# Performance work log

Hardware: AMD Instinct MI355X
Metric: run time of the kernel (lower is better)

## Reference

```python
import jax, jax.numpy as jnp
import numpy as np

B, N, D, H = 4, 512, 3, 128


def _linear_params(key, fan_in, fan_out):
    kw, kb = jax.random.split(key)
    lim = 1.0 / np.sqrt(fan_in)
    W = jax.random.uniform(kw, (fan_in, fan_out), jnp.float32, -lim, lim)
    b = jax.random.uniform(kb, (fan_out,), jnp.float32, -lim, lim)
    return W, b


def setup_inputs() -> dict:
    key = jax.random.key(0)
    ks = jax.random.split(key, 9)
    x = jax.random.normal(ks[0], (B, N, D), jnp.float32)
    Ws1, bs1 = _linear_params(ks[1], D, H)   # make_features.single
    Wp1, bp1 = _linear_params(ks[2], D, H)   # make_features.pair
    Wc1s, bc1s = _linear_params(ks[3], H, H)  # combine1.single
    Wc1p, bc1p = _linear_params(ks[4], H, H)  # combine1.pair
    Wpl, bpl = _linear_params(ks[5], H, H)    # pair_lin
    Wc2s, bc2s = _linear_params(ks[6], H, D)  # combine2.single (random, not zero-init, to exercise full graph)
    Wc2p, bc2p = _linear_params(ks[7], H, D)  # combine2.pair
    Wskip = -jnp.eye(D, dtype=jnp.float32)    # skip.weight init = -I (applied as x @ Wskip.T)
    return dict(x=x, Ws1=Ws1, bs1=bs1, Wp1=Wp1, bp1=bp1,
                Wc1s=Wc1s, bc1s=bc1s, Wc1p=Wc1p, bc1p=bc1p,
                Wpl=Wpl, bpl=bpl, Wc2s=Wc2s, bc2s=bc2s,
                Wc2p=Wc2p, bc2p=bc2p, Wskip=Wskip)


def reference(x, Ws1, bs1, Wp1, bp1, Wc1s, bc1s, Wc1p, bc1p,
              Wpl, bpl, Wc2s, bc2s, Wc2p, bc2p, Wskip):
    ht = lambda v: jnp.clip(v, -1.0, 1.0)  # Hardtanh
    n = x.shape[-2]
    # pairs[..., i, j, :] = x[j] - x[i]
    pairs = x[..., None, :, :] - x[..., :, None, :]          # [B, N, N, D]
    s = ht(x @ Ws1 + bs1)                                    # [B, N, H]
    p = ht(pairs @ Wp1 + bp1)                                # [B, N, N, H]
    # combine1: single(s) + pair(p).sum(dim=-3); sum-then-matmul is identical math, cheaper
    s = s @ Wc1s + bc1s + (p.sum(axis=-3) @ Wc1p + n * bc1p)  # [B, N, H]
    p = p @ Wpl + bpl                                         # [B, N, N, H]
    s = ht(s)
    p = ht(p)
    out = s @ Wc2s + bc2s + (p.sum(axis=-3) @ Wc2p + n * bc2p)  # [B, N, D]
    out = out + x @ Wskip.T                                     # skip (bias-free linear)
    return out
```

## Files before the change

kernel.cpp:

```cpp
#include <hip/hip_runtime.h>
#include <hip/hip_bf16.h>


typedef float f32x4 __attribute__((ext_vector_type(4)));
typedef __bf16 bf16x8 __attribute__((ext_vector_type(8)));

union PKU { uint4 u; bf16x8 v; };

__device__ __forceinline__ float ht1(float v) { return __builtin_amdgcn_fmed3f(v, -1.0f, 1.0f); }
__device__ __forceinline__ unsigned f2bf(float f) {
    unsigned u = __float_as_uint(f);
    u += 0x7FFF + ((u >> 16) & 1);
    return u >> 16;
}
__device__ __forceinline__ unsigned cvtpk(float a, float b) {
    unsigned r;
    asm("v_cvt_pk_bf16_f32 %0, %1, %2" : "=v"(r) : "v"(a), "v"(b));
    return r;
}

__global__ void prep_kernel(const float* __restrict__ x, const float* __restrict__ Wp1,
                            const float* __restrict__ Wpl,
                            const float* __restrict__ Wc1s, const float* __restrict__ Wc1p,
                            float* __restrict__ q, unsigned* __restrict__ wsBf,
                            float* __restrict__ wt1s, float* __restrict__ wt1p) {
    int gid = blockIdx.x * 256 + threadIdx.x;
    if (blockIdx.x < 1024) {
        int h = gid & 127, n = gid >> 7;
        const float* xp = x + n * 3;
        q[gid] = xp[0] * Wp1[h] + xp[1] * Wp1[128 + h] + xp[2] * Wp1[256 + h];
    } else if (blockIdx.x < 1056) {
        int g = gid - 1024 * 256;
        int w  = g & 3;
        int l  = (g >> 2) & 63;
        int fi = g >> 8;
        int wn = fi >> 4, nf = (fi >> 2) & 3, kf = fi & 3;
        int n = wn * 64 + nf * 16 + (l & 15);
        int k = kf * 32 + (l >> 4) * 8 + w * 2;
        unsigned lo = f2bf(Wpl[k * 128 + n]);
        unsigned hi = f2bf(Wpl[(k + 1) * 128 + n]);
        wsBf[g] = lo | (hi << 16);
    } else {
        int g = gid - 1056 * 256;
        int m = g >> 14;
        int e = g & 16383;
        int h = e >> 7, k = e & 127;
        if (m) wt1p[e] = Wc1p[k * 128 + h];
        else   wt1s[e] = Wc1s[k * 128 + h];
    }
}

__global__ __launch_bounds__(256, 2) void pair_kernel(
    const float* __restrict__ q, const unsigned* __restrict__ wsBf,
    const float* __restrict__ bp1, const float* __restrict__ bpl,
    const float* __restrict__ x,
    const float* __restrict__ Ws1, const float* __restrict__ bs1,
    const float* __restrict__ wt1s, const float* __restrict__ wt1p,
    const float* __restrict__ bc1s, const float* __restrict__ bc1p,
    const float* __restrict__ Wc2s, const float* __restrict__ bc2s,
    const float* __restrict__ Wc2p, const float* __restrict__ bc2p,
    const float* __restrict__ Wskip,
    float* __restrict__ out)
{
    __shared__ uint4 A_lds[2][2048];
    __shared__ float ps1[16][128];
    __shared__ float ps2[2][128];
    __shared__ float s1l[128], p1l[128], s2p[2][128], red[8];

    const int tid  = threadIdx.x;
    const int lane = tid & 63;
    const int wid  = tid >> 6;
    const int wm = wid >> 1, wn = wid & 1;
    const int bj = blockIdx.x;
    const int b  = bj >> 9;
    const float* __restrict__ qb = q + (b << 9) * 128;

    bf16x8 Bf[4][4];
    #pragma unroll
    for (int nf = 0; nf < 4; ++nf)
        #pragma unroll
        for (int kf = 0; kf < 4; ++kf) {
            PKU t;
            t.u = *(const uint4*)(wsBf + ((((wn << 4) | (nf << 2) | kf) << 6) | lane) * 4);
            Bf[nf][kf] = t.v;
        }

    const int c = tid & 15, rb = tid >> 4;
    float qjb[8];
    {
        const float* qj = q + bj * 128 + c * 8;
        #pragma unroll
        for (int e = 0; e < 8; ++e) qjb[e] = qj[e] + bp1[c * 8 + e];
    }
    float bplv[4];
    #pragma unroll
    for (int nf = 0; nf < 4; ++nf) bplv[nf] = bpl[wn * 64 + nf * 16 + (lane & 15)];

    float psum1r[8] = {0, 0, 0, 0, 0, 0, 0, 0};
    f32x4 acc[4][4];
    float colsum[4] = {0, 0, 0, 0};
    const f32x4 zf = (f32x4){0.f, 0.f, 0.f, 0.f};

    for (int ch = 0; ch < 4; ++ch) {
        uint4* __restrict__ Ab = A_lds[ch & 1];
        #pragma unroll
        for (int u = 0; u < 8; ++u) {
            const int r = (u << 4) | rb;
            const int i = (ch << 7) | r;
            const float4 q0 = *(const float4*)(qb + i * 128 + c * 8);
            const float4 q1 = *(const float4*)(qb + i * 128 + c * 8 + 4);
            float p[8];
            p[0] = ht1(qjb[0] - q0.x); p[1] = ht1(qjb[1] - q0.y);
            p[2] = ht1(qjb[2] - q0.z); p[3] = ht1(qjb[3] - q0.w);
            p[4] = ht1(qjb[4] - q1.x); p[5] = ht1(qjb[5] - q1.y);
            p[6] = ht1(qjb[6] - q1.z); p[7] = ht1(qjb[7] - q1.w);
            #pragma unroll
            for (int e = 0; e < 8; ++e) psum1r[e] += p[e];
            uint4 pk;
            pk.x = cvtpk(p[0], p[1]);
            pk.y = cvtpk(p[2], p[3]);
            pk.z = cvtpk(p[4], p[5]);
            pk.w = cvtpk(p[6], p[7]);
            unsigned addr = (r << 8) | (c << 4);
            addr ^= ((r & 7) << 4);
            Ab[addr >> 4] = pk;
        }
        __syncthreads();
        #pragma unroll
        for (int kf = 0; kf < 4; ++kf) {
            bf16x8 Af[4];
            #pragma unroll
            for (int mf = 0; mf < 4; ++mf) {
                const int row = wm * 64 + mf * 16 + (lane & 15);
                unsigned addr = (row << 8) + (kf << 6) + ((lane >> 4) << 4);
                addr ^= ((row & 7) << 4);
                PKU t; t.u = Ab[addr >> 4];
                Af[mf] = t.v;
            }
            #pragma unroll
            for (int mf = 0; mf < 4; ++mf)
                #pragma unroll
                for (int nf = 0; nf < 4; ++nf)
                    acc[mf][nf] = __builtin_amdgcn_mfma_f32_16x16x32_bf16(
                        Af[mf], Bf[nf][kf], kf == 0 ? zf : acc[mf][nf], 0, 0, 0);
        }
        #pragma unroll
        for (int mf = 0; mf < 4; ++mf)
            #pragma unroll
            for (int nf = 0; nf < 4; ++nf) {
                f32x4 a = acc[mf][nf];
                colsum[nf] += ht1(a.x + bplv[nf]) + ht1(a.y + bplv[nf])
                            + ht1(a.z + bplv[nf]) + ht1(a.w + bplv[nf]);
            }
    }

    *(float4*)(&ps1[rb][c * 8])     = make_float4(psum1r[0], psum1r[1], psum1r[2], psum1r[3]);
    *(float4*)(&ps1[rb][c * 8 + 4]) = make_float4(psum1r[4], psum1r[5], psum1r[6], psum1r[7]);
    #pragma unroll
    for (int nf = 0; nf < 4; ++nf) {
        float v = colsum[nf];
        v += __shfl_xor(v, 16);
        v += __shfl_xor(v, 32);
        if (lane < 16) ps2[wm][wn * 64 + nf * 16 + lane] = v;
    }
    __syncthreads();

    const int h = tid & 127;
    if (tid < 128) {
        float s = 0.f;
        #pragma unroll
        for (int r2 = 0; r2 < 16; ++r2) s += ps1[r2][tid];
        p1l[tid] = s;
        const float* xj = x + bj * 3;
        s1l[tid] = ht1(xj[0] * Ws1[tid] + xj[1] * Ws1[128 + tid] + xj[2] * Ws1[256 + tid] + bs1[tid]);
    }
    __syncthreads();

    {
        const int half = tid >> 7;
        const float* w1 = wt1s + h * 128 + half * 64;
        const float* w2 = wt1p + h * 128 + half * 64;
        float a2 = 0.f;
        #pragma unroll
        for (int k = 0; k < 64; k += 4) {
            float4 wa = *(const float4*)(w1 + k);
            float4 wb = *(const float4*)(w2 + k);
            const int kk = half * 64 + k;
            a2 += wa.x * s1l[kk] + wa.y * s1l[kk + 1] + wa.z * s1l[kk + 2] + wa.w * s1l[kk + 3];
            a2 += wb.x * p1l[kk] + wb.y * p1l[kk + 1] + wb.z * p1l[kk + 2] + wb.w * p1l[kk + 3];
        }
        s2p[half][h] = a2;
    }
    __syncthreads();

    if (tid < 128) {
        float s3 = ht1(s2p[0][tid] + s2p[1][tid] + bc1s[tid] + 512.0f * bc1p[tid]);
        float pp = ps2[0][tid] + ps2[1][tid];
        float c0 = s3 * Wc2s[tid * 3 + 0] + pp * Wc2p[tid * 3 + 0];
        float c1 = s3 * Wc2s[tid * 3 + 1] + pp * Wc2p[tid * 3 + 1];
        float c2 = s3 * Wc2s[tid * 3 + 2] + pp * Wc2p[tid * 3 + 2];
        #pragma unroll
        for (int off = 32; off > 0; off >>= 1) {
            c0 += __shfl_down(c0, off);
            c1 += __shfl_down(c1, off);
            c2 += __shfl_down(c2, off);
        }
        if (lane == 0) {
            red[wid * 3 + 0] = c0;
            red[wid * 3 + 1] = c1;
            red[wid * 3 + 2] = c2;
        }
    }
    __syncthreads();
    if (tid < 3) {
        const float* xj = x + bj * 3;
        float o = red[tid] + red[3 + tid];
        o += bc2s[tid] + 512.0f * bc2p[tid];
        o += xj[0] * Wskip[tid * 3 + 0] + xj[1] * Wskip[tid * 3 + 1] + xj[2] * Wskip[tid * 3 + 2];
        out[bj * 3 + tid] = o;
    }
}

extern "C" void kernel_launch(void* const* d_in, const int* in_sizes, int n_in,
                              void* d_out, int out_size, void* d_ws, size_t ws_size,
                              hipStream_t stream) {
    const float* x    = (const float*)d_in[0];
    const float* Ws1  = (const float*)d_in[1];
    const float* bs1  = (const float*)d_in[2];
    const float* Wp1  = (const float*)d_in[3];
    const float* bp1  = (const float*)d_in[4];
    const float* Wc1s = (const float*)d_in[5];
    const float* bc1s = (const float*)d_in[6];
    const float* Wc1p = (const float*)d_in[7];
    const float* bc1p = (const float*)d_in[8];
    const float* Wpl  = (const float*)d_in[9];
    const float* bpl  = (const float*)d_in[10];
    const float* Wc2s = (const float*)d_in[11];
    const float* bc2s = (const float*)d_in[12];
    const float* Wc2p = (const float*)d_in[13];
    const float* bc2p = (const float*)d_in[14];
    const float* Wskip= (const float*)d_in[15];

    float*    q    = (float*)d_ws;
    unsigned* wsBf = (unsigned*)((char*)d_ws + (1 << 20));
    float*    wt1s = (float*)((char*)d_ws + (1 << 20) + 32768);
    float*    wt1p = wt1s + 16384;

    prep_kernel<<<1184, 256, 0, stream>>>(x, Wp1, Wpl, Wc1s, Wc1p, q, wsBf, wt1s, wt1p);
    pair_kernel<<<2048, 256, 0, stream>>>(q, wsBf, bp1, bpl, x, Ws1, bs1,
                                          wt1s, wt1p, bc1s, bc1p,
                                          Wc2s, bc2s, Wc2p, bc2p, Wskip,
                                          (float*)d_out);
}
```

Before: 179.0 us.

## Single-buffer LDS in a union and raise pair kernel occupancy to four blocks

Shrinks LDS use of the pair kernel by replacing the double-buffered A tile with one buffer, adding a barrier after the MFMA reads so the next chunk can overwrite it. The reduction scratch arrays now share the same LDS space through a union, and the per-row psum partials are first reduced across lanes with shuffles so only four rows remain. Launch bounds are raised from 2 to 4 blocks per CU. The aim is more resident waves to hide latency, in exchange for an extra barrier per chunk and a tighter register budget that may cause spills.

```diff
diff --git a/kernel.cpp b/kernel.cpp
--- a/kernel.cpp
+++ b/kernel.cpp
@@ -50,7 +50,7 @@
     }
 }
 
-__global__ __launch_bounds__(256, 2) void pair_kernel(
+__global__ __launch_bounds__(256, 4) void pair_kernel(
     const float* __restrict__ q, const unsigned* __restrict__ wsBf,
     const float* __restrict__ bp1, const float* __restrict__ bpl,
     const float* __restrict__ x,
@@ -62,10 +62,16 @@
     const float* __restrict__ Wskip,
     float* __restrict__ out)
 {
-    __shared__ uint4 A_lds[2][2048];
-    __shared__ float ps1[16][128];
-    __shared__ float ps2[2][128];
-    __shared__ float s1l[128], p1l[128], s2p[2][128], red[8];
+    __shared__ union {
+        uint4 A[2048];
+        struct {
+            float ps1[4][128];
+            float ps2[2][128];
+            float s1l[128], p1l[128];
+            float s2p[2][128];
+            float red[8];
+        } t;
+    } sm;
 
     const int tid  = threadIdx.x;
     const int lane = tid & 63;
@@ -102,7 +108,6 @@
     const f32x4 zf = (f32x4){0.f, 0.f, 0.f, 0.f};
 
     for (int ch = 0; ch < 4; ++ch) {
-        uint4* __restrict__ Ab = A_lds[ch & 1];
         #pragma unroll
         for (int u = 0; u < 8; ++u) {
             const int r = (u << 4) | rb;
@@ -123,7 +128,7 @@
             pk.w = cvtpk(p[6], p[7]);
             unsigned addr = (r << 8) | (c << 4);
             addr ^= ((r & 7) << 4);
-            Ab[addr >> 4] = pk;
+            sm.A[addr >> 4] = pk;
         }
         __syncthreads();
         #pragma unroll
@@ -134,7 +139,7 @@
                 const int row = wm * 64 + mf * 16 + (lane & 15);
                 unsigned addr = (row << 8) + (kf << 6) + ((lane >> 4) << 4);
                 addr ^= ((row & 7) << 4);
-                PKU t; t.u = Ab[addr >> 4];
+                PKU t; t.u = sm.A[addr >> 4];
                 Af[mf] = t.v;
             }
             #pragma unroll
@@ -144,6 +149,7 @@
                     acc[mf][nf] = __builtin_amdgcn_mfma_f32_16x16x32_bf16(
                         Af[mf], Bf[nf][kf], kf == 0 ? zf : acc[mf][nf], 0, 0, 0);
         }
+        __syncthreads();
         #pragma unroll
         for (int mf = 0; mf < 4; ++mf)
             #pragma unroll
@@ -154,25 +160,29 @@
             }
     }
 
-    *(float4*)(&ps1[rb][c * 8])     = make_float4(psum1r[0], psum1r[1], psum1r[2], psum1r[3]);
-    *(float4*)(&ps1[rb][c * 8 + 4]) = make_float4(psum1r[4], psum1r[5], psum1r[6], psum1r[7]);
+    #pragma unroll
+    for (int e = 0; e < 8; ++e) {
+        psum1r[e] += __shfl_xor(psum1r[e], 16);
+        psum1r[e] += __shfl_xor(psum1r[e], 32);
+    }
+    if ((lane >> 4) == 0) {
+        *(float4*)(&sm.t.ps1[wid][c * 8])     = make_float4(psum1r[0], psum1r[1], psum1r[2], psum1r[3]);
+        *(float4*)(&sm.t.ps1[wid][c * 8 + 4]) = make_float4(psum1r[4], psum1r[5], psum1r[6], psum1r[7]);
+    }
     #pragma unroll
     for (int nf = 0; nf < 4; ++nf) {
         float v = colsum[nf];
         v += __shfl_xor(v, 16);
         v += __shfl_xor(v, 32);
-        if (lane < 16) ps2[wm][wn * 64 + nf * 16 + lane] = v;
+        if (lane < 16) sm.t.ps2[wm][wn * 64 + nf * 16 + lane] = v;
     }
     __syncthreads();
 
     const int h = tid & 127;
     if (tid < 128) {
-        float s = 0.f;
-        #pragma unroll
-        for (int r2 = 0; r2 < 16; ++r2) s += ps1[r2][tid];
-        p1l[tid] = s;
+        sm.t.p1l[tid] = sm.t.ps1[0][tid] + sm.t.ps1[1][tid] + sm.t.ps1[2][tid] + sm.t.ps1[3][tid];
         const float* xj = x + bj * 3;
-        s1l[tid] = ht1(xj[0] * Ws1[tid] + xj[1] * Ws1[128 + tid] + xj[2] * Ws1[256 + tid] + bs1[tid]);
+        sm.t.s1l[tid] = ht1(xj[0] * Ws1[tid] + xj[1] * Ws1[128 + tid] + xj[2] * Ws1[256 + tid] + bs1[tid]);
     }
     __syncthreads();
 
@@ -186,16 +196,16 @@
             float4 wa = *(const float4*)(w1 + k);
             float4 wb = *(const float4*)(w2 + k);
             const int kk = half * 64 + k;
-            a2 += wa.x * s1l[kk] + wa.y * s1l[kk + 1] + wa.z * s1l[kk + 2] + wa.w * s1l[kk + 3];
-            a2 += wb.x * p1l[kk] + wb.y * p1l[kk + 1] + wb.z * p1l[kk + 2] + wb.w * p1l[kk + 3];
-        }
-        s2p[half][h] = a2;
+            a2 += wa.x * sm.t.s1l[kk] + wa.y * sm.t.s1l[kk + 1] + wa.z * sm.t.s1l[kk + 2] + wa.w * sm.t.s1l[kk + 3];
+            a2 += wb.x * sm.t.p1l[kk] + wb.y * sm.t.p1l[kk + 1] + wb.z * sm.t.p1l[kk + 2] + wb.w * sm.t.p1l[kk + 3];
+        }
+        sm.t.s2p[half][h] = a2;
     }
     __syncthreads();
 
     if (tid < 128) {
-        float s3 = ht1(s2p[0][tid] + s2p[1][tid] + bc1s[tid] + 512.0f * bc1p[tid]);
-        float pp = ps2[0][tid] + ps2[1][tid];
+        float s3 = ht1(sm.t.s2p[0][tid] + sm.t.s2p[1][tid] + bc1s[tid] + 512.0f * bc1p[tid]);
+        float pp = sm.t.ps2[0][tid] + sm.t.ps2[1][tid];
         float c0 = s3 * Wc2s[tid * 3 + 0] + pp * Wc2p[tid * 3 + 0];
         float c1 = s3 * Wc2s[tid * 3 + 1] + pp * Wc2p[tid * 3 + 1];
         float c2 = s3 * Wc2s[tid * 3 + 2] + pp * Wc2p[tid * 3 + 2];
@@ -206,15 +216,15 @@
             c2 += __shfl_down(c2, off);
         }
         if (lane == 0) {
-            red[wid * 3 + 0] = c0;
-            red[wid * 3 + 1] = c1;
-            red[wid * 3 + 2] = c2;
+            sm.t.red[wid * 3 + 0] = c0;
+            sm.t.red[wid * 3 + 1] = c1;
+            sm.t.red[wid * 3 + 2] = c2;
         }
     }
     __syncthreads();
     if (tid < 3) {
         const float* xj = x + bj * 3;
-        float o = red[tid] + red[3 + tid];
+        float o = sm.t.red[tid] + sm.t.red[3 + tid];
         o += bc2s[tid] + 512.0f * bc2p[tid];
         o += xj[0] * Wskip[tid * 3 + 0] + xj[1] * Wskip[tid * 3 + 1] + xj[2] * Wskip[tid * 3 + 2];
         out[bj * 3 + tid] = o;
@@ -241,13 +251,13 @@
     const float* bc2p = (const float*)d_in[14];
     const float* Wskip= (const float*)d_in[15];
 
-    float*    q    = (float*)d_ws;
+    float*    qv   = (float*)d_ws;
     unsigned* wsBf = (unsigned*)((char*)d_ws + (1 << 20));
     float*    wt1s = (float*)((char*)d_ws + (1 << 20) + 32768);
     float*    wt1p = wt1s + 16384;
 
-    prep_kernel<<<1184, 256, 0, stream>>>(x, Wp1, Wpl, Wc1s, Wc1p, q, wsBf, wt1s, wt1p);
-    pair_kernel<<<2048, 256, 0, stream>>>(q, wsBf, bp1, bpl, x, Ws1, bs1,
+    prep_kernel<<<1184, 256, 0, stream>>>(x, Wp1, Wpl, Wc1s, Wc1p, qv, wsBf, wt1s, wt1p);
+    pair_kernel<<<2048, 256, 0, stream>>>(qv, wsBf, bp1, bpl, x, Ws1, bs1,
                                           wt1s, wt1p, bc1s, bc1p,
                                           Wc2s, bc2s, Wc2p, bc2p, Wskip,
                                           (float*)d_out);
```

Result: slower. 317.4 us (+77.4%).

## Build MFMA A-fragments directly in registers, removing LDS staging of pair features

Applied to the files above, without the earlier changes.

The pair-feature tile used to be written to shared memory as bf16 and read back as MFMA A operands, with block-wide barriers between chunks. Now each lane computes its own A fragment directly in the MFMA operand layout from q rows and feeds the bf16 MFMA without going through LDS, looping over 16-row tiles. This removes the LDS traffic, the swizzled stores and loads, and the per-chunk __syncthreads. In exchange, both wn waves in a pair recompute the same hardtanh and pack work, register pressure rises from the 4x8 qjb and psum arrays, and the first-layer row sums now need a shuffle reduction.

```diff
diff --git a/kernel.cpp b/kernel.cpp
--- a/kernel.cpp
+++ b/kernel.cpp
@@ -62,15 +62,18 @@
     const float* __restrict__ Wskip,
     float* __restrict__ out)
 {
-    __shared__ uint4 A_lds[2][2048];
-    __shared__ float ps1[16][128];
-    __shared__ float ps2[2][128];
-    __shared__ float s1l[128], p1l[128], s2p[2][128], red[8];
+    __shared__ float ps1s[2][128];
+    __shared__ float ps2s[2][128];
+    __shared__ float s1l[128], p1l[128];
+    __shared__ float s2p[2][128];
+    __shared__ float red[8];
 
     const int tid  = threadIdx.x;
     const int lane = tid & 63;
     const int wid  = tid >> 6;
     const int wm = wid >> 1, wn = wid & 1;
+    const int lr = lane & 15;
+    const int ls = lane >> 4;
     const int bj = blockIdx.x;
     const int b  = bj >> 9;
     const float* __restrict__ qb = q + (b << 9) * 128;
@@ -85,92 +88,107 @@
             Bf[nf][kf] = t.v;
         }
 
-    const int c = tid & 15, rb = tid >> 4;
-    float qjb[8];
-    {
-        const float* qj = q + bj * 128 + c * 8;
-        #pragma unroll
-        for (int e = 0; e < 8; ++e) qjb[e] = qj[e] + bp1[c * 8 + e];
-    }
-    float bplv[4];
-    #pragma unroll
-    for (int nf = 0; nf < 4; ++nf) bplv[nf] = bpl[wn * 64 + nf * 16 + (lane & 15)];
-
-    float psum1r[8] = {0, 0, 0, 0, 0, 0, 0, 0};
-    f32x4 acc[4][4];
+    float qjb[4][8];
+    #pragma unroll
+    for (int kf = 0; kf < 4; ++kf) {
+        const float4 a0 = *(const float4*)(q + bj * 128 + kf * 32 + ls * 8);
+        const float4 a1 = *(const float4*)(q + bj * 128 + kf * 32 + ls * 8 + 4);
+        const float4 b0 = *(const float4*)(bp1 + kf * 32 + ls * 8);
+        const float4 b1 = *(const float4*)(bp1 + kf * 32 + ls * 8 + 4);
+        qjb[kf][0] = a0.x + b0.x; qjb[kf][1] = a0.y + b0.y;
+        qjb[kf][2] = a0.z + b0.z; qjb[kf][3] = a0.w + b0.w;
+        qjb[kf][4] = a1.x + b1.x; qjb[kf][5] = a1.y + b1.y;
+        qjb[kf][6] = a1.z + b1.z; qjb[kf][7] = a1.w + b1.w;
+    }
+    float bplv4[4];
+    #pragma unroll
+    for (int nf = 0; nf < 4; ++nf) bplv4[nf] = bpl[wn * 64 + nf * 16 + lr];
+
+    float psum1r[4][8];
+    #pragma unroll
+    for (int kf = 0; kf < 4; ++kf)
+        #pragma unroll
+        for (int e = 0; e < 8; ++e) psum1r[kf][e] = 0.f;
     float colsum[4] = {0, 0, 0, 0};
     const f32x4 zf = (f32x4){0.f, 0.f, 0.f, 0.f};
 
-    for (int ch = 0; ch < 4; ++ch) {
-        uint4* __restrict__ Ab = A_lds[ch & 1];
-        #pragma unroll
-        for (int u = 0; u < 8; ++u) {
-            const int r = (u << 4) | rb;
-            const int i = (ch << 7) | r;
-            const float4 q0 = *(const float4*)(qb + i * 128 + c * 8);
-            const float4 q1 = *(const float4*)(qb + i * 128 + c * 8 + 4);
+    for (int t = 0; t < 16; ++t) {
+        const int g = wm + 2 * t;
+        const int i = (g << 4) | lr;
+        const float* __restrict__ qrow = qb + i * 128 + ls * 8;
+
+        float4 qv[4][2];
+        #pragma unroll
+        for (int kf = 0; kf < 4; ++kf) {
+            qv[kf][0] = *(const float4*)(qrow + kf * 32);
+            qv[kf][1] = *(const float4*)(qrow + kf * 32 + 4);
+        }
+
+        f32x4 acc0 = zf, acc1 = zf, acc2 = zf, acc3 = zf;
+        #pragma unroll
+        for (int kf = 0; kf < 4; ++kf) {
             float p[8];
-            p[0] = ht1(qjb[0] - q0.x); p[1] = ht1(qjb[1] - q0.y);
-            p[2] = ht1(qjb[2] - q0.z); p[3] = ht1(qjb[3] - q0.w);
-            p[4] = ht1(qjb[4] - q1.x); p[5] = ht1(qjb[5] - q1.y);
-            p[6] = ht1(qjb[6] - q1.z); p[7] = ht1(qjb[7] - q1.w);
+            p[0] = ht1(qjb[kf][0] - qv[kf][0].x);
+            p[1] = ht1(qjb[kf][1] - qv[kf][0].y);
+            p[2] = ht1(qjb[kf][2] - qv[kf][0].z);
+            p[3] = ht1(qjb[kf][3] - qv[kf][0].w);
+            p[4] = ht1(qjb[kf][4] - qv[kf][1].x);
+            p[5] = ht1(qjb[kf][5] - qv[kf][1].y);
+            p[6] = ht1(qjb[kf][6] - qv[kf][1].z);
+            p[7] = ht1(qjb[kf][7] - qv[kf][1].w);
+            if (wn == 0) {
+                #pragma unroll
+                for (int e = 0; e < 8; ++e) psum1r[kf][e] += p[e];
+            }
+            PKU t4;
+            t4.u.x = cvtpk(p[0], p[1]);
+            t4.u.y = cvtpk(p[2], p[3]);
+            t4.u.z = cvtpk(p[4], p[5]);
+            t4.u.w = cvtpk(p[6], p[7]);
+            const bf16x8 Af = t4.v;
+            acc0 = __builtin_amdgcn_mfma_f32_16x16x32_bf16(Af, Bf[0][kf], acc0, 0, 0, 0);
+            acc1 = __builtin_amdgcn_mfma_f32_16x16x32_bf16(Af, Bf[1][kf], acc1, 0, 0, 0);
+            acc2 = __builtin_amdgcn_mfma_f32_16x16x32_bf16(Af, Bf[2][kf], acc2, 0, 0, 0);
+            acc3 = __builtin_amdgcn_mfma_f32_16x16x32_bf16(Af, Bf[3][kf], acc3, 0, 0, 0);
+        }
+        colsum[0] += ht1(acc0.x + bplv4[0]) + ht1(acc0.y + bplv4[0]) + ht1(acc0.z + bplv4[0]) + ht1(acc0.w + bplv4[0]);
+        colsum[1] += ht1(acc1.x + bplv4[1]) + ht1(acc1.y + bplv4[1]) + ht1(acc1.z + bplv4[1]) + ht1(acc1.w + bplv4[1]);
+        colsum[2] += ht1(acc2.x + bplv4[2]) + ht1(acc2.y + bplv4[2]) + ht1(acc2.z + bplv4[2]) + ht1(acc2.w + bplv4[2]);
+        colsum[3] += ht1(acc3.x + bplv4[3]) + ht1(acc3.y + bplv4[3]) + ht1(acc3.z + bplv4[3]) + ht1(acc3.w + bplv4[3]);
+    }
+
+    if (wn == 0) {
+        #pragma unroll
+        for (int kf = 0; kf < 4; ++kf)
             #pragma unroll
-            for (int e = 0; e < 8; ++e) psum1r[e] += p[e];
-            uint4 pk;
-            pk.x = cvtpk(p[0], p[1]);
-            pk.y = cvtpk(p[2], p[3]);
-            pk.z = cvtpk(p[4], p[5]);
-            pk.w = cvtpk(p[6], p[7]);
-            unsigned addr = (r << 8) | (c << 4);
-            addr ^= ((r & 7) << 4);
-            Ab[addr >> 4] = pk;
-        }
-        __syncthreads();
-        #pragma unroll
-        for (int kf = 0; kf < 4; ++kf) {
-            bf16x8 Af[4];
+            for (int e = 0; e < 8; ++e) {
+                float v = psum1r[kf][e];
+                v += __shfl_xor(v, 1);
+                v += __shfl_xor(v, 2);
+                v += __shfl_xor(v, 4);
+                v += __shfl_xor(v, 8);
+                psum1r[kf][e] = v;
+            }
+        if (lr == 0) {
             #pragma unroll
-            for (int mf = 0; mf < 4; ++mf) {
-                const int row = wm * 64 + mf * 16 + (lane & 15);
-                unsigned addr = (row << 8) + (kf << 6) + ((lane >> 4) << 4);
-                addr ^= ((row & 7) << 4);
-                PKU t; t.u = Ab[addr >> 4];
-                Af[mf] = t.v;
-            }
-            #pragma unroll
-            for (int mf = 0; mf < 4; ++mf)
+            for (int kf = 0; kf < 4; ++kf)
                 #pragma unroll
-                for (int nf = 0; nf < 4; ++nf)
-                    acc[mf][nf] = __builtin_amdgcn_mfma_f32_16x16x32_bf16(
-                        Af[mf], Bf[nf][kf], kf == 0 ? zf : acc[mf][nf], 0, 0, 0);
-        }
-        #pragma unroll
-        for (int mf = 0; mf < 4; ++mf)
-            #pragma unroll
-            for (int nf = 0; nf < 4; ++nf) {
-                f32x4 a = acc[mf][nf];
-                colsum[nf] += ht1(a.x + bplv[nf]) + ht1(a.y + bplv[nf])
-                            + ht1(a.z + bplv[nf]) + ht1(a.w + bplv[nf]);
-            }
-    }
-
-    *(float4*)(&ps1[rb][c * 8])     = make_float4(psum1r[0], psum1r[1], psum1r[2], psum1r[3]);
-    *(float4*)(&ps1[rb][c * 8 + 4]) = make_float4(psum1r[4], psum1r[5], psum1r[6], psum1r[7]);
+                for (int e = 0; e < 8; ++e)
+                    ps1s[wm][kf * 32 + ls * 8 + e] = psum1r[kf][e];
+        }
+    }
     #pragma unroll
     for (int nf = 0; nf < 4; ++nf) {
         float v = colsum[nf];
         v += __shfl_xor(v, 16);
         v += __shfl_xor(v, 32);
-        if (lane < 16) ps2[wm][wn * 64 + nf * 16 + lane] = v;
+        if (lane < 16) ps2s[wm][wn * 64 + nf * 16 + lane] = v;
     }
     __syncthreads();
 
     const int h = tid & 127;
     if (tid < 128) {
-        float s = 0.f;
-        #pragma unroll
-        for (int r2 = 0; r2 < 16; ++r2) s += ps1[r2][tid];
-        p1l[tid] = s;
+        p1l[tid] = ps1s[0][tid] + ps1s[1][tid];
         const float* xj = x + bj * 3;
         s1l[tid] = ht1(xj[0] * Ws1[tid] + xj[1] * Ws1[128 + tid] + xj[2] * Ws1[256 + tid] + bs1[tid]);
     }
@@ -195,7 +213,7 @@
 
     if (tid < 128) {
         float s3 = ht1(s2p[0][tid] + s2p[1][tid] + bc1s[tid] + 512.0f * bc1p[tid]);
-        float pp = ps2[0][tid] + ps2[1][tid];
+        float pp = ps2s[0][tid] + ps2s[1][tid];
         float c0 = s3 * Wc2s[tid * 3 + 0] + pp * Wc2p[tid * 3 + 0];
         float c1 = s3 * Wc2s[tid * 3 + 1] + pp * Wc2p[tid * 3 + 1];
         float c2 = s3 * Wc2s[tid * 3 + 2] + pp * Wc2p[tid * 3 + 2];
@@ -241,13 +259,13 @@
     const float* bc2p = (const float*)d_in[14];
     const float* Wskip= (const float*)d_in[15];
 
-    float*    q    = (float*)d_ws;
+    float*    qv   = (float*)d_ws;
     unsigned* wsBf = (unsigned*)((char*)d_ws + (1 << 20));
     float*    wt1s = (float*)((char*)d_ws + (1 << 20) + 32768);
     float*    wt1p = wt1s + 16384;
 
-    prep_kernel<<<1184, 256, 0, stream>>>(x, Wp1, Wpl, Wc1s, Wc1p, q, wsBf, wt1s, wt1p);
-    pair_kernel<<<2048, 256, 0, stream>>>(q, wsBf, bp1, bpl, x, Ws1, bs1,
+    prep_kernel<<<1184, 256, 0, stream>>>(x, Wp1, Wpl, Wc1s, Wc1p, qv, wsBf, wt1s, wt1p);
+    pair_kernel<<<2048, 256, 0, stream>>>(qv, wsBf, bp1, bpl, x, Ws1, bs1,
                                           wt1s, wt1p, bc1s, bc1p,
                                           Wc2s, bc2s, Wc2p, bc2p, Wskip,
                                           (float*)d_out);
```

New measurement: 240.5 us. +34.4%, slower.
